# Optimization experiments

Hardware: AMD Instinct MI355X
Metric: run time of the kernel (lower is better)

## Reference

```python
import jax, jax.numpy as jnp
import numpy as np

B, T, C = 2, 2048, 1024
HS = 64              # head_size
H = C // HS          # 16 heads
DW, DA, DV, DG = 64, 64, 32, 160   # RWKV-7 LoRA dims for C=1024
FFN = 4 * C
GN_EPS = 64e-5       # ln_x GroupNorm eps from source


def _layernorm(h, w, b, eps=1e-5):
    mu = jnp.mean(h, axis=-1, keepdims=True)
    var = jnp.mean(jnp.square(h - mu), axis=-1, keepdims=True)
    return (h - mu) * jax.lax.rsqrt(var + eps) * w + b


def _time_shift_delta(h):
    # ZeroPad2d((0,0,1,-1))(h) - h : previous-token delta
    return jnp.pad(h, ((0, 0), (1, 0), (0, 0)))[:, :-1, :] - h


def _wkv7_scan(decay, r, k, v, a, b, S0):
    # all inputs [B,T,H,N]; state S [B,H,N_v,N_k]
    # S_t = S_{t-1} * diag(decay_t) + (S_{t-1} @ a_t) b_t^T + v_t k_t^T ; y_t = S_t @ r_t
    def step(S, inp):
        w_t, r_t, k_t, v_t, a_t, b_t = inp
        S = S * w_t[:, :, None, :]
        sa = jnp.einsum('bhij,bhj->bhi', S, a_t)
        S = S + sa[..., None] * b_t[:, :, None, :] + v_t[..., None] * k_t[:, :, None, :]
        y = jnp.einsum('bhij,bhj->bhi', S, r_t)
        return S, y
    seq = tuple(jnp.moveaxis(t, 1, 0) for t in (decay, r, k, v, a, b))
    S_last, y = jax.lax.scan(step, S0, seq)
    return jnp.moveaxis(y, 0, 1), S_last


def _block_forward(x, v_first, init_state, ln1_w, ln1_b, ln2_w, ln2_b,
                   x_r, x_w, x_k, x_v, x_a, x_g, w0, w1, w2, a0, a1, a2,
                   v0, v1, v2, g1, g2, k_k, k_a, r_k, W_r, W_k, W_v, W_o,
                   ln_x_w, ln_x_b, mix_k_ffn, W_key_ffn, W_val_ffn):
    # ---- time-mix (RWKV_Tmix_x070), layer_idx = 1 ----
    xn = _layernorm(x, ln1_w, ln1_b)
    xx = _time_shift_delta(xn)
    xr = xn + xx * x_r
    xw = xn + xx * x_w
    xk = xn + xx * x_k
    xv = xn + xx * x_v
    xa = xn + xx * x_a
    xg = xn + xx * x_g
    r = xr @ W_r.T
    w = -jax.nn.softplus(-(w0 + jnp.tanh(xw @ w1) @ w2)) - 0.5   # w <= -0.5
    k = xk @ W_k.T
    v = xv @ W_v.T
    v = v + (v_first - v) * jax.nn.sigmoid(v0 + (xv @ v1) @ v2)  # layer_idx > 0 path
    a = jax.nn.sigmoid(a0 + (xa @ a1) @ a2)
    g = jax.nn.sigmoid(xg @ g1) @ g2
    kk = (k * k_k).reshape(B, T, H, HS)
    kk = kk / jnp.maximum(jnp.linalg.norm(kk, axis=-1, keepdims=True), 1e-12)
    k = k * (1.0 + (a - 1.0) * k_a)
    r4 = r.reshape(B, T, H, HS)
    k4 = k.reshape(B, T, H, HS)
    v4 = v.reshape(B, T, H, HS)
    a4 = a.reshape(B, T, H, HS)
    decay = jnp.exp(w).reshape(B, T, H, HS)
    y, S_last = _wkv7_scan(decay, r4, k4, v4, -kk, kk * a4, init_state)
    # GroupNorm(H groups, eps=64e-5) over C, per (b,t)
    mu = jnp.mean(y, axis=-1, keepdims=True)
    var = jnp.mean(jnp.square(y - mu), axis=-1, keepdims=True)
    y = ((y - mu) * jax.lax.rsqrt(var + GN_EPS)).reshape(B, T, C) * ln_x_w + ln_x_b
    y = y + (jnp.sum(r4 * k4 * r_k, axis=-1, keepdims=True) * v4).reshape(B, T, C)
    x = x + (y * g) @ W_o.T
    # ---- channel-mix (RWKV_CMix_x070) ----
    xn2 = _layernorm(x, ln2_w, ln2_b)
    kf = xn2 + _time_shift_delta(xn2) * mix_k_ffn
    kf = jnp.square(jax.nn.relu(kf @ W_key_ffn.T))
    x = x + kf @ W_val_ffn.T
    return x, v_first


def setup_inputs():
    key = jax.random.key(0)
    ks = iter(jax.random.split(key, 40))
    def nrm(shape, s):
        return jax.random.normal(next(ks), shape, dtype=jnp.float32) * s
    def uni(shape, lo=0.0, hi=1.0):
        return jax.random.uniform(next(ks), shape, dtype=jnp.float32, minval=lo, maxval=hi)
    return {
        'x': nrm((B, T, C), 1.0),
        'v_first': nrm((B, T, C), 1.0),
        'init_state': jnp.zeros((B, H, HS, HS), jnp.float32),
        'ln1_w': jnp.ones((C,), jnp.float32), 'ln1_b': jnp.zeros((C,), jnp.float32),
        'ln2_w': jnp.ones((C,), jnp.float32), 'ln2_b': jnp.zeros((C,), jnp.float32),
        'x_r': uni((C,)), 'x_w': uni((C,)), 'x_k': uni((C,)),
        'x_v': uni((C,)), 'x_a': uni((C,)), 'x_g': uni((C,)),
        'w0': uni((C,), -6.5, -1.5),
        'w1': nrm((C, DW), 0.02), 'w2': nrm((DW, C), 0.02),
        'a0': jnp.zeros((C,), jnp.float32),
        'a1': nrm((C, DA), 0.02), 'a2': nrm((DA, C), 0.02),
        'v0': jnp.ones((C,), jnp.float32),
        'v1': nrm((C, DV), 0.02), 'v2': nrm((DV, C), 0.02),
        'g1': nrm((C, DG), 0.02), 'g2': nrm((DG, C), 0.02),
        'k_k': 0.85 * jnp.ones((C,), jnp.float32),
        'k_a': jnp.ones((C,), jnp.float32),
        'r_k': nrm((H, HS), 0.02),
        'W_r': nrm((C, C), 0.02), 'W_k': nrm((C, C), 0.02),
        'W_v': nrm((C, C), 0.02), 'W_o': nrm((C, C), 0.02),
        'ln_x_w': jnp.ones((C,), jnp.float32), 'ln_x_b': jnp.zeros((C,), jnp.float32),
        'mix_k_ffn': uni((C,)),
        'W_key_ffn': nrm((FFN, C), 0.02), 'W_val_ffn': nrm((C, FFN), 0.02),
    }


def reference(x, v_first, init_state, ln1_w, ln1_b, ln2_w, ln2_b,
              x_r, x_w, x_k, x_v, x_a, x_g, w0, w1, w2, a0, a1, a2,
              v0, v1, v2, g1, g2, k_k, k_a, r_k, W_r, W_k, W_v, W_o,
              ln_x_w, ln_x_b, mix_k_ffn, W_key_ffn, W_val_ffn):
    return _block_forward(x, v_first, init_state, ln1_w, ln1_b, ln2_w, ln2_b,
                          x_r, x_w, x_k, x_v, x_a, x_g, w0, w1, w2, a0, a1, a2,
                          v0, v1, v2, g1, g2, k_k, k_a, r_k, W_r, W_k, W_v, W_o,
                          ln_x_w, ln_x_b, mix_k_ffn, W_key_ffn, W_val_ffn)
```

## Files before the change

kernel.cpp:

```cpp
#include <hip/hip_runtime.h>
#include <math.h>

#define Bb 2
#define Tt 2048
#define Cc 1024
#define Hh 16
#define BT 4096
#define FFNd 4096
#define CH 16
#define CL 128
#define WU 32
#define BIGN 3456
#define BIGK 2048
#define LORAK 320
#define BIGW 4096

typedef __attribute__((ext_vector_type(8))) short bf16x8;
typedef __attribute__((ext_vector_type(4))) float f32x4;
typedef unsigned short u16;

__device__ __forceinline__ float sgm(float x){ return 1.0f/(1.0f+expf(-x)); }

template<int MAXM>
__device__ __forceinline__ float redgrp(float v){
  #pragma unroll
  for (int m=1; m<=MAXM; m<<=1) v += __shfl_xor(v, m, 64);
  return v;
}

template<int CTRL>
__device__ __forceinline__ float dppadd(float v){
  union { float f; int i; } u, r;
  u.f = v;
  r.i = __builtin_amdgcn_update_dpp(u.i, u.i, CTRL, 0xf, 0xf, true);
  return v + r.f;
}
__device__ __forceinline__ float red16(float v){
  v = dppadd<0xB1>(v);
  v = dppadd<0x4E>(v);
  v = dppadd<0x141>(v);
  v = dppadd<0x140>(v);
  return v;
}

__device__ __forceinline__ unsigned pack_bf16(float a, float b){
  unsigned ua = __builtin_bit_cast(unsigned, a);
  unsigned ub = __builtin_bit_cast(unsigned, b);
  ua = (ua + 0x7FFFu + ((ua>>16)&1u)) >> 16;
  ub = (ub + 0x7FFFu + ((ub>>16)&1u)) >> 16;
  return ua | (ub<<16);
}
__device__ __forceinline__ u16 bf16_1(float a){
  unsigned ua = __builtin_bit_cast(unsigned, a);
  return (u16)((ua + 0x7FFFu + ((ua>>16)&1u)) >> 16);
}

__device__ __forceinline__ void gload16(const void* g, void* l){
  __builtin_amdgcn_global_load_lds(
    (const __attribute__((address_space(1))) unsigned int*)g,
    (__attribute__((address_space(3))) unsigned int*)l, 16, 0, 0);
}

__device__ __forceinline__ void cvt8(const float* __restrict__ in,
    u16* __restrict__ out, size_t i){
  float4 a = ((const float4*)in)[2*i];
  float4 b = ((const float4*)in)[2*i+1];
  uint4 o = {pack_bf16(a.x,a.y), pack_bf16(a.z,a.w),
             pack_bf16(b.x,b.y), pack_bf16(b.z,b.w)};
  ((uint4*)out)[i] = o;
}
__global__ __launch_bounds__(256) void cvtall_kernel(
    const float* __restrict__ wo, u16* __restrict__ wob,
    const float* __restrict__ wk, u16* __restrict__ wkb,
    const float* __restrict__ wv, u16* __restrict__ wvb,
    const float* __restrict__ csrc, float* __restrict__ cdst) {
  size_t i = (size_t)blockIdx.x*256 + threadIdx.x;
  const size_t NA = (size_t)Cc*Cc/8;
  const size_t NB = (size_t)FFNd*Cc/8;
  if (i < NA) cvt8(wo, wob, i);
  else if (i < NA+NB) cvt8(wk, wkb, i-NA);
  else if (i < NA+2*NB) cvt8(wv, wvb, i-NA-NB);
  else {
    size_t j = i - NA - 2*NB;
    float4 a = ((const float4*)csrc)[2*j];
    float4 b = ((const float4*)csrc)[2*j+1];
    ((float4*)cdst)[2*j] = a;
    ((float4*)cdst)[2*j+1] = b;
  }
}

__global__ __launch_bounds__(256) void packW_kernel(const float* __restrict__ Wr,
    const float* __restrict__ Wk, const float* __restrict__ Wv,
    const float* __restrict__ xr, const float* __restrict__ xk,
    const float* __restrict__ xv, u16* __restrict__ out) {
  int which = blockIdx.y;
  const float* W   = which==0 ? Wr : (which==1 ? Wk : Wv);
  const float* mix = which==0 ? xr : (which==1 ? xk : xv);
  u16* o = out + (size_t)which*1024*BIGK;
  int n = blockIdx.x;
  int c0 = threadIdx.x*8;
  int ks = c0 & 1023;
  const float* src = W + (size_t)n*Cc + ks;
  float4 a = *(const float4*)src;
  float4 b = *(const float4*)(src+4);
  if (c0 >= 1024){
    float4 m0 = *(const float4*)(mix + ks);
    float4 m1 = *(const float4*)(mix + ks + 4);
    a.x*=m0.x; a.y*=m0.y; a.z*=m0.z; a.w*=m0.w;
    b.x*=m1.x; b.y*=m1.y; b.z*=m1.z; b.w*=m1.w;
  }
  uint4 ov = {pack_bf16(a.x,a.y), pack_bf16(a.z,a.w),
              pack_bf16(b.x,b.y), pack_bf16(b.z,b.w)};
  *(uint4*)(o + (size_t)n*BIGK + c0) = ov;
}

__global__ __launch_bounds__(256) void packL_kernel(const float* __restrict__ w1,
    const float* __restrict__ a1, const float* __restrict__ v1,
    const float* __restrict__ g1, const float* __restrict__ x_w,
    const float* __restrict__ x_a, const float* __restrict__ x_v,
    const float* __restrict__ x_g, u16* __restrict__ out) {
  int bid = blockIdx.x;
  const float* W1; const float* mix; int D, d, nbase;
  if (bid < 64)       { W1=w1; mix=x_w; D=64;  d=bid;     nbase=3072; }
  else if (bid < 128) { W1=a1; mix=x_a; D=64;  d=bid-64;  nbase=3136; }
  else if (bid < 160) { W1=v1; mix=x_v; D=32;  d=bid-128; nbase=3200; }
  else                { W1=g1; mix=x_g; D=160; d=bid-160; nbase=3232; }
  int k0 = threadIdx.x*8;
  float v[8];
  #pragma unroll
  for (int q=0;q<8;++q){
    int kk = k0+q;
    int ks = kk & 1023;
    float t = W1[(size_t)ks*D + d];
    if (kk >= 1024) t *= mix[ks];
    v[q] = t;
  }
  uint4 o = {pack_bf16(v[0],v[1]), pack_bf16(v[2],v[3]),
             pack_bf16(v[4],v[5]), pack_bf16(v[6],v[7])};
  *(uint4*)(out + (size_t)(nbase+d)*BIGK + k0) = o;
}

__global__ __launch_bounds__(320) void packW2_kernel(const float* __restrict__ w2,
    const float* __restrict__ a2, const float* __restrict__ v2,
    const float* __restrict__ g2, u16* __restrict__ out) {
  int n = blockIdx.x; int k = threadIdx.x;
  int which = n >> 10, col = n & 1023;
  float v = 0.f;
  if (which==0)      { if (k < 64)              v = w2[(size_t)k*Cc + col]; }
  else if (which==1) { if (k >= 64 && k < 128)  v = a2[(size_t)(k-64)*Cc + col]; }
  else if (which==2) { if (k >= 128 && k < 160) v = v2[(size_t)(k-128)*Cc + col]; }
  else               { if (k >= 160)            v = g2[(size_t)(k-160)*Cc + col]; }
  out[(size_t)n*LORAK + k] = bf16_1(v);
}

__global__ __launch_bounds__(320) void actcvt_kernel(const float* __restrict__ m,
    u16* __restrict__ loraAct) {
  int i = blockIdx.x; int cc = threadIdx.x;
  float v = m[(size_t)i*BIGN + 3072 + cc];
  if (cc < 64) v = tanhf(v);
  else if (cc >= 160) v = sgm(v);
  loraAct[(size_t)i*LORAK + cc] = bf16_1(v);
}

__global__ __launch_bounds__(256) void lnmix1_kernel(const float* __restrict__ x,
    const float* __restrict__ w, const float* __restrict__ b,
    u16* __restrict__ bigA) {
  int rowg = blockIdx.x; int t = rowg & (Tt-1);
  int tid = threadIdx.x;
  size_t off = (size_t)rowg*Cc + tid*4;
  float4 vc = *(const float4*)(x + off);
  float4 vp = {0.f,0.f,0.f,0.f};
  if (t) vp = *(const float4*)(x + off - Cc);
  float sc = vc.x+vc.y+vc.z+vc.w;
  float qc = vc.x*vc.x+vc.y*vc.y+vc.z*vc.z+vc.w*vc.w;
  float sp = vp.x+vp.y+vp.z+vp.w;
  float qp = vp.x*vp.x+vp.y*vp.y+vp.z*vp.z+vp.w*vp.w;
  sc = redgrp<32>(sc); qc = redgrp<32>(qc);
  sp = redgrp<32>(sp); qp = redgrp<32>(qp);
  __shared__ float rbuf[4][4];
  int lane = tid & 63, wv = tid >> 6;
  if (lane==0){ rbuf[wv][0]=sc; rbuf[wv][1]=qc; rbuf[wv][2]=sp; rbuf[wv][3]=qp; }
  __syncthreads();
  sc = rbuf[0][0]+rbuf[1][0]+rbuf[2][0]+rbuf[3][0];
  qc = rbuf[0][1]+rbuf[1][1]+rbuf[2][1]+rbuf[3][1];
  sp = rbuf[0][2]+rbuf[1][2]+rbuf[2][2]+rbuf[3][2];
  qp = rbuf[0][3]+rbuf[1][3]+rbuf[2][3]+rbuf[3][3];
  float muc = sc*(1.0f/Cc), mup = sp*(1.0f/Cc);
  float rnc = rsqrtf(qc*(1.0f/Cc) - muc*muc + 1e-5f);
  float rnp = rsqrtf(qp*(1.0f/Cc) - mup*mup + 1e-5f);
  float4 w4 = *(const float4*)(w + tid*4);
  float4 b4 = *(const float4*)(b + tid*4);
  float vcl[4]={vc.x,vc.y,vc.z,vc.w};
  float vpl[4]={vp.x,vp.y,vp.z,vp.w};
  float wl[4]={w4.x,w4.y,w4.z,w4.w};
  float bl[4]={b4.x,b4.y,b4.z,b4.w};
  float xnc[4], xx[4];
  #pragma unroll
  for (int q=0;q<4;++q){
    xnc[q] = (vcl[q]-muc)*rnc*wl[q] + bl[q];
    float xnp = t ? ((vpl[q]-mup)*rnp*wl[q] + bl[q]) : 0.0f;
    xx[q] = xnp - xnc[q];
  }
  size_t ab = (size_t)rowg*BIGK + tid*4;
  uint2 p0 = {pack_bf16(xnc[0],xnc[1]), pack_bf16(xnc[2],xnc[3])};
  uint2 p1 = {pack_bf16(xx[0],xx[1]),   pack_bf16(xx[2],xx[3])};
  *(uint2*)(bigA + ab) = p0;
  *(uint2*)(bigA + ab + 1024) = p1;
}

__global__ __launch_bounds__(256) void lnmix2_kernel(const float* __restrict__ x,
    const float* __restrict__ w, const float* __restrict__ b,
    const float* __restrict__ mixk, u16* __restrict__ outb) {
  int rowg = blockIdx.x; int t = rowg & (Tt-1);
  int tid = threadIdx.x;
  size_t off = (size_t)rowg*Cc + tid*4;
  float4 vc = *(const float4*)(x + off);
  float4 vp = {0.f,0.f,0.f,0.f};
  if (t) vp = *(const float4*)(x + off - Cc);
  float sc = vc.x+vc.y+vc.z+vc.w;
  float qc = vc.x*vc.x+vc.y*vc.y+vc.z*vc.z+vc.w*vc.w;
  float sp = vp.x+vp.y+vp.z+vp.w;
  float qp = vp.x*vp.x+vp.y*vp.y+vp.z*vp.z+vp.w*vp.w;
  sc = redgrp<32>(sc); qc = redgrp<32>(qc);
  sp = redgrp<32>(sp); qp = redgrp<32>(qp);
  __shared__ float rbuf[4][4];
  int lane = tid & 63, wv = tid >> 6;
  if (lane==0){ rbuf[wv][0]=sc; rbuf[wv][1]=qc; rbuf[wv][2]=sp; rbuf[wv][3]=qp; }
  __syncthreads();
  sc = rbuf[0][0]+rbuf[1][0]+rbuf[2][0]+rbuf[3][0];
  qc = rbuf[0][1]+rbuf[1][1]+rbuf[2][1]+rbuf[3][1];
  sp = rbuf[0][2]+rbuf[1][2]+rbuf[2][2]+rbuf[3][2];
  qp = rbuf[0][3]+rbuf[1][3]+rbuf[2][3]+rbuf[3][3];
  float muc = sc*(1.0f/Cc), mup = sp*(1.0f/Cc);
  float rnc = rsqrtf(qc*(1.0f/Cc) - muc*muc + 1e-5f);
  float rnp = rsqrtf(qp*(1.0f/Cc) - mup*mup + 1e-5f);
  float4 w4 = *(const float4*)(w + tid*4);
  float4 b4 = *(const float4*)(b + tid*4);
  float4 m = *(const float4*)(mixk + tid*4);
  float vcl[4]={vc.x,vc.y,vc.z,vc.w};
  float vpl[4]={vp.x,vp.y,vp.z,vp.w};
  float wl[4]={w4.x,w4.y,w4.z,w4.w};
  float bl[4]={b4.x,b4.y,b4.z,b4.w};
  float ml[4]={m.x,m.y,m.z,m.w};
  float o[4];
  #pragma unroll
  for (int q=0;q<4;++q){
    float xnc = (vcl[q]-muc)*rnc*wl[q] + bl[q];
    float xnp = t ? ((vpl[q]-mup)*rnp*wl[q] + bl[q]) : 0.0f;
    o[q] = xnc + (xnp - xnc)*ml[q];
  }
  uint2 p = {pack_bf16(o[0],o[1]), pack_bf16(o[2],o[3])};
  *(uint2*)(outb + off) = p;
}

template<int MODE, int BN>
__global__ __launch_bounds__(256) void gemm_bf16(const u16* __restrict__ A,
    const u16* __restrict__ W, void* __restrict__ outv,
    const float* __restrict__ res, int M, int N, int K) {
  constexpr int NJ = BN/32;
  constexpr int NBCH = BN/32;
  __shared__ u16 As[2][128*64];
  __shared__ u16 Bs[2][BN*64];
  int tid = threadIdx.x;
  int nwg = gridDim.x;
  int q8 = nwg >> 3;
  int id = (blockIdx.x & 7)*q8 + (blockIdx.x >> 3);
  int nbx = N / BN;
  int bm = id / nbx, bn = id - bm*nbx;
  int wave = tid >> 6, lane = tid & 63;
  int wm = wave >> 1, wn = wave & 1;
  int srowA = wave*32 + (lane>>3);
  int srowB = wave*(BN/4) + (lane>>3);
  int scol = (((lane&7) ^ ((lane>>3)&7)))*8;
  const u16* Ag = A + (size_t)(bm*128 + srowA)*K + scol;
  const u16* Wg = W + (size_t)(bn*BN + srowB)*K + scol;
  int nt = K >> 6;
  f32x4 acc[4][NJ];
  f32x4 zero = {0.f,0.f,0.f,0.f};
  #pragma unroll
  for (int i=0;i<4;++i)
    #pragma unroll
    for (int j=0;j<NJ;++j) acc[i][j] = zero;

  #define STAGE(buf, t) { \
    const u16* Ag2 = Ag + (size_t)(t)*64; \
    const u16* Wg2 = Wg + (size_t)(t)*64; \
    _Pragma("unroll") \
    for (int i_=0;i_<4;++i_) \
      gload16(Ag2 + (size_t)i_*8*K, &As[buf][(wave*32+i_*8)*64]); \
    _Pragma("unroll") \
    for (int i_=0;i_<NBCH;++i_) \
      gload16(Wg2 + (size_t)i_*8*K, &Bs[buf][(wave*(BN/4)+i_*8)*64]); }

  STAGE(0, 0);
  int lrow = lane & 15, lk8 = lane >> 4;
  int r7 = lrow & 7;
  for (int t = 0; t < nt; ++t) {
    int cur = t & 1;
    if (t+1 < nt) {
      STAGE(cur^1, t+1);
      if (BN == 128) asm volatile("s_waitcnt vmcnt(8)\n\ts_barrier" ::: "memory");
      else           asm volatile("s_waitcnt vmcnt(6)\n\ts_barrier" ::: "memory");
    } else {
      asm volatile("s_waitcnt vmcnt(0)\n\ts_barrier" ::: "memory");
    }
    #pragma unroll
    for (int kk2 = 0; kk2 < 2; ++kk2) {
      int sl = ((kk2*4 + lk8) ^ r7) * 8;
      bf16x8 af[4], bfr[NJ];
      #pragma unroll
      for (int i=0;i<4;++i)
        af[i] = *(const bf16x8*)&As[cur][(wm*64 + i*16 + lrow)*64 + sl];
      #pragma unroll
      for (int j=0;j<NJ;++j)
        bfr[j] = *(const bf16x8*)&Bs[cur][(wn*(BN/2) + j*16 + lrow)*64 + sl];
      #pragma unroll
      for (int i=0;i<4;++i)
        #pragma unroll
        for (int j=0;j<NJ;++j)
          acc[i][j] = __builtin_amdgcn_mfma_f32_16x16x32_bf16(af[i], bfr[j], acc[i][j], 0, 0, 0);
    }
    asm volatile("s_barrier" ::: "memory");
  }
  #undef STAGE
  float* outf = (float*)outv;
  u16* outb = (u16*)outv;
  int crow4 = (lane>>4)*4, ccol = lane & 15;
  #pragma unroll
  for (int i=0;i<4;++i){
    #pragma unroll
    for (int j=0;j<NJ;++j){
      int gr = bm*128 + wm*64 + i*16 + crow4;
      int gc = bn*BN + wn*(BN/2) + j*16 + ccol;
      #pragma unroll
      for (int q=0;q<4;++q){
        float v = acc[i][j][q];
        size_t o = (size_t)(gr+q)*N + gc;
        if (MODE==1) { v += res[o]; outf[o] = v; }
        else if (MODE==2) { v = fmaxf(v, 0.f); outb[o] = bf16_1(v*v); }
        else outf[o] = v;
      }
    }
  }
}

__global__ __launch_bounds__(256) void prep_kernel(
    const float* __restrict__ kraw, const float* __restrict__ dw,
    const float* __restrict__ da, const float* __restrict__ dv,
    const float* __restrict__ vraw, const float* __restrict__ vfirst,
    const float* __restrict__ w0, const float* __restrict__ a0,
    const float* __restrict__ v0, const float* __restrict__ k_k,
    const float* __restrict__ k_a,
    float* __restrict__ decay, float* __restrict__ kfin, float* __restrict__ vfin,
    float* __restrict__ Ak, float* __restrict__ Bk) {
  int row = blockIdx.x; int tid = threadIdx.x; int c = tid*4;
  size_t off = (size_t)row*Cc + c;
  size_t offw = (size_t)row*BIGN + c;
  size_t offd = (size_t)row*BIGW + c;
  float4 kr = *(const float4*)(kraw+offw);
  float4 vr = *(const float4*)(vraw+offw);
  float4 w4 = *(const float4*)(dw+offd);
  float4 A4 = *(const float4*)(da+offd);
  float4 V4 = *(const float4*)(dv+offd);
  float4 vf = *(const float4*)(vfirst+off);
  float4 w04 = *(const float4*)(w0+c);
  float4 a04 = *(const float4*)(a0+c);
  float4 v04 = *(const float4*)(v0+c);
  float4 kk4 = *(const float4*)(k_k+c);
  float4 ka4 = *(const float4*)(k_a+c);
  float krl[4]={kr.x,kr.y,kr.z,kr.w};
  float dwl[4]={w4.x,w4.y,w4.z,w4.w};
  float dal[4]={A4.x,A4.y,A4.z,A4.w};
  float dvl[4]={V4.x,V4.y,V4.z,V4.w};
  float vrl[4]={vr.x,vr.y,vr.z,vr.w};
  float vfl[4]={vf.x,vf.y,vf.z,vf.w};
  float w0l[4]={w04.x,w04.y,w04.z,w04.w};
  float a0l[4]={a04.x,a04.y,a04.z,a04.w};
  float v0l[4]={v04.x,v04.y,v04.z,v04.w};
  float kkl[4]={kk4.x,kk4.y,kk4.z,kk4.w};
  float kal[4]={ka4.x,ka4.y,ka4.z,ka4.w};
  float av[4], dec[4], vv[4], kp[4], kf[4];
  float ss = 0.f;
  #pragma unroll
  for (int q=0;q<4;++q){
    av[q] = sgm(a0l[q] + dal[q]);
    dec[q] = 0.60653065971263342f * sgm(w0l[q] + dwl[q]);
    float sv = sgm(v0l[q] + dvl[q]);
    vv[q] = vrl[q] + (vfl[q]-vrl[q])*sv;
    kp[q] = krl[q]*kkl[q];
    ss += kp[q]*kp[q];
    kf[q] = krl[q]*(1.0f + (av[q]-1.0f)*kal[q]);
  }
  ss = redgrp<8>(ss);
  float inv = 1.0f / fmaxf(sqrtf(ss), 1e-12f);
  float4 o;
  o.x=dec[0];o.y=dec[1];o.z=dec[2];o.w=dec[3];  *(float4*)(decay+off)=o;
  o.x=kf[0]; o.y=kf[1]; o.z=kf[2]; o.w=kf[3];   *(float4*)(kfin+off)=o;
  o.x=vv[0]; o.y=vv[1]; o.z=vv[2]; o.w=vv[3];   *(float4*)(vfin+off)=o;
  o.x=-kp[0]*inv; o.y=-kp[1]*inv; o.z=-kp[2]*inv; o.w=-kp[3]*inv; *(float4*)(Ak+off)=o;
  o.x=kp[0]*inv*av[0]; o.y=kp[1]*inv*av[1]; o.z=kp[2]*inv*av[2]; o.w=kp[3]*inv*av[3];
  *(float4*)(Bk+off)=o;
}

__global__ __launch_bounds__(512) void wkv_kernel(
    const float* __restrict__ decay, const float* __restrict__ Ak,
    const float* __restrict__ Bk, const float* __restrict__ kfin,
    const float* __restrict__ r_, const float* __restrict__ vfin,
    const float* __restrict__ S0, float* __restrict__ y) {
  __shared__ float lds[2][6][CH][64];
  int bid = blockIdx.x;
  int bh = bid & 31, c = bid >> 5;
  int bb = bh >> 4, h = bh & 15;
  int tid = threadIdx.x;
  int wave = tid >> 6, lane = tid & 63;
  int rg = tid >> 4;
  int bj = tid & 15, j0 = bj*4;
  int r0 = rg, r1 = rg + 32;
  float Sa_[4] = {0.f,0.f,0.f,0.f};
  float Sb_[4] = {0.f,0.f,0.f,0.f};
  if (c == 0) {
    float4 t0 = *(const float4*)(S0 + (size_t)bh*4096 + r0*64 + j0);
    float4 t1 = *(const float4*)(S0 + (size_t)bh*4096 + r1*64 + j0);
    Sa_[0]=t0.x; Sa_[1]=t0.y; Sa_[2]=t0.z; Sa_[3]=t0.w;
    Sb_[0]=t1.x; Sb_[1]=t1.y; Sb_[2]=t1.z; Sb_[3]=t1.w;
  }
  size_t seqb = (size_t)bb*Tt;
  int t0g = (c==0) ? 0 : (c*CL - WU);
  int NPH = (c==0) ? (CL/CH) : ((CL+WU)/CH);
  int phE = (c==0) ? 0 : (WU/CH);
  int lhi = lane >> 4, llo4 = (lane & 15)*4;

  #define WST1(buf, stepb, arr, base, ldv) { \
    const float* gp_ = (base) + (size_t)(seqb + (size_t)(stepb) + lhi)*(ldv) + h*64 + llo4; \
    _Pragma("unroll") \
    for (int p_=0; p_<4; ++p_) \
      gload16(gp_ + (size_t)p_*4*(ldv), &lds[buf][arr][p_*4][0]); }
  #define WSTAGE(buf, stepb) { \
    if (wave==0)      { WST1(buf, stepb, 0, decay, Cc) } \
    else if (wave==1) { WST1(buf, stepb, 1, Ak, Cc) } \
    else if (wave==2) { WST1(buf, stepb, 2, Bk, Cc) } \
    else if (wave==3) { WST1(buf, stepb, 3, kfin, Cc) } \
    else if (wave==4) { WST1(buf, stepb, 4, r_, BIGN) } \
    else if (wave==5) { WST1(buf, stepb, 5, vfin, Cc) } }

  WSTAGE(0, t0g);
  for (int ph = 0; ph < NPH; ++ph) {
    int cur = ph & 1;
    if (ph+1 < NPH) {
      WSTAGE(cur^1, t0g + (ph+1)*CH);
      asm volatile("s_waitcnt vmcnt(4)\n\ts_barrier" ::: "memory");
    } else {
      asm volatile("s_waitcnt vmcnt(0)\n\ts_barrier" ::: "memory");
    }
    bool emit = (ph >= phE);
    const float* L0 = &lds[cur][0][0][0];
    #pragma unroll
    for (int s = 0; s < CH; ++s) {
      const float* bp = L0 + s*64;
      float4 d4 = *(const float4*)(bp + 0*CH*64 + j0);
      float4 a4 = *(const float4*)(bp + 1*CH*64 + j0);
      float4 b4 = *(const float4*)(bp + 2*CH*64 + j0);
      float4 k4 = *(const float4*)(bp + 3*CH*64 + j0);
      float4 r4 = *(const float4*)(bp + 4*CH*64 + j0);
      float v0 = bp[5*CH*64 + r0];
      float v1 = bp[5*CH*64 + r1];
      Sa_[0]*=d4.x; Sa_[1]*=d4.y; Sa_[2]*=d4.z; Sa_[3]*=d4.w;
      Sb_[0]*=d4.x; Sb_[1]*=d4.y; Sb_[2]*=d4.z; Sb_[3]*=d4.w;
      float sa0 = fmaf(Sa_[0],a4.x, Sa_[1]*a4.y) + fmaf(Sa_[2],a4.z, Sa_[3]*a4.w);
      float sa1 = fmaf(Sb_[0],a4.x, Sb_[1]*a4.y) + fmaf(Sb_[2],a4.z, Sb_[3]*a4.w);
      sa0 = red16(sa0);
      sa1 = red16(sa1);
      Sa_[0]=fmaf(v0,k4.x,Sa_[0]); Sa_[1]=fmaf(v0,k4.y,Sa_[1]);
      Sa_[2]=fmaf(v0,k4.z,Sa_[2]); Sa_[3]=fmaf(v0,k4.w,Sa_[3]);
      Sa_[0]=fmaf(sa0,b4.x,Sa_[0]); Sa_[1]=fmaf(sa0,b4.y,Sa_[1]);
      Sa_[2]=fmaf(sa0,b4.z,Sa_[2]); Sa_[3]=fmaf(sa0,b4.w,Sa_[3]);
      Sb_[0]=fmaf(v1,k4.x,Sb_[0]); Sb_[1]=fmaf(v1,k4.y,Sb_[1]);
      Sb_[2]=fmaf(v1,k4.z,Sb_[2]); Sb_[3]=fmaf(v1,k4.w,Sb_[3]);
      Sb_[0]=fmaf(sa1,b4.x,Sb_[0]); Sb_[1]=fmaf(sa1,b4.y,Sb_[1]);
      Sb_[2]=fmaf(sa1,b4.z,Sb_[2]); Sb_[3]=fmaf(sa1,b4.w,Sb_[3]);
      if (emit) {
        float y0 = fmaf(Sa_[0],r4.x, Sa_[1]*r4.y) + fmaf(Sa_[2],r4.z, Sa_[3]*r4.w);
        float y1 = fmaf(Sb_[0],r4.x, Sb_[1]*r4.y) + fmaf(Sb_[2],r4.z, Sb_[3]*r4.w);
        y0 = red16(y0);
        y1 = red16(y1);
        if (bj == 0) {
          size_t yo = (seqb + (size_t)t0g + ph*CH + s)*Cc + h*64;
          y[yo + r0] = y0;
          y[yo + r1] = y1;
        }
      }
    }
    asm volatile("s_barrier" ::: "memory");
  }
  #undef WSTAGE
  #undef WST1
}

__global__ __launch_bounds__(256) void gn_kernel(
    const float* __restrict__ y, const float* __restrict__ r_,
    const float* __restrict__ kfin, const float* __restrict__ vfin,
    const float* __restrict__ g_, const float* __restrict__ lnxw,
    const float* __restrict__ lnxb, const float* __restrict__ r_k,
    u16* __restrict__ Ao) {
  int row = blockIdx.x; int tid = threadIdx.x; int c = tid*4;
  size_t off = (size_t)row*Cc + c;
  float4 y4 = *(const float4*)(y+off);
  float s = y4.x+y4.y+y4.z+y4.w;
  float q = y4.x*y4.x+y4.y*y4.y+y4.z*y4.z+y4.w*y4.w;
  s = redgrp<8>(s); q = redgrp<8>(q);
  float mu = s*(1.0f/64.0f);
  float var = q*(1.0f/64.0f) - mu*mu;
  float rn = rsqrtf(var + 64e-5f);
  float4 rr = *(const float4*)(r_ + (size_t)row*BIGN + c);
  float4 kk = *(const float4*)(kfin+off);
  float4 vv = *(const float4*)(vfin+off);
  float4 gg = *(const float4*)(g_ + (size_t)row*BIGW + c);
  int h = tid >> 4; int hs = (tid & 15)*4;
  float4 rk = *(const float4*)(r_k + h*64 + hs);
  float dp = rr.x*kk.x*rk.x + rr.y*kk.y*rk.y + rr.z*kk.z*rk.z + rr.w*kk.w*rk.w;
  dp = redgrp<8>(dp);
  float4 w4 = *(const float4*)(lnxw+c);
  float4 b4 = *(const float4*)(lnxb+c);
  float o0 = (((y4.x-mu)*rn)*w4.x + b4.x + dp*vv.x) * gg.x;
  float o1 = (((y4.y-mu)*rn)*w4.y + b4.y + dp*vv.y) * gg.y;
  float o2 = (((y4.z-mu)*rn)*w4.z + b4.z + dp*vv.z) * gg.z;
  float o3 = (((y4.w-mu)*rn)*w4.w + b4.w + dp*vv.w) * gg.w;
  uint2 p = {pack_bf16(o0,o1), pack_bf16(o2,o3)};
  *(uint2*)(Ao + off) = p;
}

extern "C" void kernel_launch(void* const* d_in, const int* in_sizes, int n_in,
                              void* d_out, int out_size, void* d_ws, size_t ws_size,
                              hipStream_t stream) {
  const float* x      = (const float*)d_in[0];
  const float* vfirst = (const float*)d_in[1];
  const float* S0     = (const float*)d_in[2];
  const float* ln1w   = (const float*)d_in[3];
  const float* ln1b   = (const float*)d_in[4];
  const float* ln2w   = (const float*)d_in[5];
  const float* ln2b   = (const float*)d_in[6];
  const float* x_r    = (const float*)d_in[7];
  const float* x_w    = (const float*)d_in[8];
  const float* x_k    = (const float*)d_in[9];
  const float* x_v    = (const float*)d_in[10];
  const float* x_a    = (const float*)d_in[11];
  const float* x_g    = (const float*)d_in[12];
  const float* w0     = (const float*)d_in[13];
  const float* w1     = (const float*)d_in[14];
  const float* w2     = (const float*)d_in[15];
  const float* a0     = (const float*)d_in[16];
  const float* a1     = (const float*)d_in[17];
  const float* a2     = (const float*)d_in[18];
  const float* v0     = (const float*)d_in[19];
  const float* v1     = (const float*)d_in[20];
  const float* v2     = (const float*)d_in[21];
  const float* g1     = (const float*)d_in[22];
  const float* g2     = (const float*)d_in[23];
  const float* k_k    = (const float*)d_in[24];
  const float* k_a    = (const float*)d_in[25];
  const float* r_k    = (const float*)d_in[26];
  const float* W_r    = (const float*)d_in[27];
  const float* W_k    = (const float*)d_in[28];
  const float* W_v    = (const float*)d_in[29];
  const float* W_o    = (const float*)d_in[30];
  const float* lnxw   = (const float*)d_in[31];
  const float* lnxb   = (const float*)d_in[32];
  const float* mixk   = (const float*)d_in[33];
  const float* Wkey   = (const float*)d_in[34];
  const float* Wval   = (const float*)d_in[35];
  float* out = (float*)d_out;
  float* ws  = (float*)d_ws;
  const size_t U = (size_t)BT * Cc;
  float* u[14];
  for (int i=0;i<14;++i) u[i] = ws + i*U;

  u16* bigA   = (u16*)u[0];
  u16* BigB   = (u16*)u[1];
  float* bigOut = u[2];
  float* dwdavg = u[6];
  u16* W2blk  = (u16*)u[10];
  u16* loraAct= (u16*)u[11];
  float* Bk   = u[0];
  float* y_   = u[1];
  u16* gnb    = (u16*)u[10];
  u16* Wob    = (u16*)u[13];
  float* xo   = u[0];
  u16* Wkeyb  = (u16*)u[6];
  u16* cmb    = (u16*)u[7];
  u16* Wvalb  = (u16*)u[8];
  u16* midb   = (u16*)u[2];

  dim3 b256(256);
  packW_kernel<<<dim3(Cc,3), b256, 0, stream>>>(W_r, W_k, W_v, x_r, x_k, x_v, BigB);
  packL_kernel<<<320, b256, 0, stream>>>(w1, a1, v1, g1, x_w, x_a, x_v, x_g, BigB);
  packW2_kernel<<<BIGW, dim3(320), 0, stream>>>(w2, a2, v2, g2, W2blk);
  lnmix1_kernel<<<BT, b256, 0, stream>>>(x, ln1w, ln1b, bigA);
  gemm_bf16<0,128><<<(BT/128)*(BIGN/128), b256, 0, stream>>>(bigA, BigB, bigOut, nullptr, BT, BIGN, BIGK);
  actcvt_kernel<<<BT, dim3(320), 0, stream>>>(bigOut, loraAct);
  gemm_bf16<0,128><<<(BT/128)*(BIGW/128), b256, 0, stream>>>(loraAct, W2blk, dwdavg, nullptr, BT, BIGW, LORAK);
  prep_kernel<<<BT, b256, 0, stream>>>(bigOut+1024, dwdavg, dwdavg+1024, dwdavg+2048,
      bigOut+2048, vfirst, w0, a0, v0, k_k, k_a, u[10], u[11], u[12], u[13], Bk);
  wkv_kernel<<<32*(Tt/CL), dim3(512), 0, stream>>>(u[10], u[13], Bk, u[11], bigOut, u[12], S0, y_);
  gn_kernel<<<BT, b256, 0, stream>>>(y_, bigOut, u[11], u[12], dwdavg+3072, lnxw, lnxb, r_k, gnb);
  cvtall_kernel<<<(Cc*Cc + FFNd*Cc*2 + BT*Cc)/2048, b256, 0, stream>>>(
      W_o, Wob, Wkey, Wkeyb, Wval, Wvalb, vfirst, out + (size_t)BT*Cc);
  gemm_bf16<1,64><<<(BT/128)*(Cc/64), b256, 0, stream>>>(gnb, Wob, xo, x, BT, Cc, Cc);
  lnmix2_kernel<<<BT, b256, 0, stream>>>(xo, ln2w, ln2b, mixk, cmb);
  gemm_bf16<2,128><<<(BT/128)*(FFNd/128), b256, 0, stream>>>(cmb, Wkeyb, midb, nullptr, BT, FFNd, Cc);
  gemm_bf16<1,64><<<(BT/128)*(Cc/64), b256, 0, stream>>>(midb, Wvalb, out, xo, BT, Cc, FFNd);
}
```

Before: 394.2 us.

## Add 256x256-tile 8-wave GEMM for fused projection and FFN key GEMMs

Introduces a 512-thread GEMM kernel with 256x256 output tiles and double-buffered LDS. Its schedule interleaves global prefetch of the next K tile with MFMA quadrants, separated by barriers, and raises wave priority around the MFMA blocks. The fused r/k/v/LoRA projection and the FFN key GEMM switch to this kernel to get more data reuse per tile and fewer global loads. To fit the 256-wide tiles, the fused projection width is padded up, which adds extra padded compute, and each GEMM now launches fewer, larger workgroups.

```diff
diff --git a/kernel.cpp b/kernel.cpp
--- a/kernel.cpp
+++ b/kernel.cpp
@@ -10,7 +10,7 @@
 #define CH 16
 #define CL 128
 #define WU 32
-#define BIGN 3456
+#define BIGN 3584
 #define BIGK 2048
 #define LORAK 320
 #define BIGW 4096
@@ -251,6 +251,133 @@
   }
   uint2 p = {pack_bf16(o[0],o[1]), pack_bf16(o[2],o[3])};
   *(uint2*)(outb + off) = p;
+}
+
+template<int MODE>
+__global__ __launch_bounds__(512) void gemm8(const u16* __restrict__ A,
+    const u16* __restrict__ W, void* __restrict__ outv, int M, int N, int K) {
+  __shared__ u16 As[2*2*128*64];
+  __shared__ u16 Bs[2*2*128*64];
+  int tid = threadIdx.x;
+  int nwg = gridDim.x;
+  int q8 = nwg >> 3;
+  int id = (blockIdx.x & 7)*q8 + (blockIdx.x >> 3);
+  int nbx = N >> 8;
+  int bm = id / nbx, bn = id - bm*nbx;
+  int wave = tid >> 6, lane = tid & 63;
+  int wm = wave >> 2, wn = wave & 3;
+  int lrow = lane & 15, lk8 = lane >> 4;
+  int r7 = lrow & 7;
+  int bhlf = wn >> 1;
+  int chb = (wn & 1)*64;
+  int sw = wave*16;
+  int sl8 = lane >> 3;
+  int schunk = ((lane & 7) ^ sl8) * 8;
+  int nt = K >> 6;
+  int lastJ = (nt >> 1) - 1;
+  f32x4 acc[8][4];
+  f32x4 zero = {0.f,0.f,0.f,0.f};
+  #pragma unroll
+  for (int i=0;i<8;++i)
+    #pragma unroll
+    for (int j=0;j<4;++j) acc[i][j] = zero;
+
+  #define STGA(T, h) { \
+    const u16* s_ = A + (size_t)(bm*256 + (h)*128 + sw + sl8)*K + (size_t)(T)*64 + schunk; \
+    char* d_ = (char*)As + (((T)&1)*32768 + (h)*16384) + wave*2048; \
+    gload16(s_, d_); \
+    gload16(s_ + (size_t)8*K, d_ + 1024); }
+  #define STGB(T, h) { \
+    const u16* s_ = W + (size_t)(bn*256 + (h)*128 + sw + sl8)*K + (size_t)(T)*64 + schunk; \
+    char* d_ = (char*)Bs + (((T)&1)*32768 + (h)*16384) + wave*2048; \
+    gload16(s_, d_); \
+    gload16(s_ + (size_t)8*K, d_ + 1024); }
+  #define RDA(T, mh) { \
+    _Pragma("unroll") \
+    for (int ii=0; ii<4; ++ii) \
+      _Pragma("unroll") \
+      for (int kk=0; kk<2; ++kk) \
+        Am[ii][kk] = *(const bf16x8*)&As[((T)&1)*16384 + wm*8192 + \
+          ((mh)*64 + ii*16 + lrow)*64 + ((kk*4 + lk8) ^ r7)*8]; }
+  #define RDB(T, nh, Bd) { \
+    _Pragma("unroll") \
+    for (int jj=0; jj<2; ++jj) \
+      _Pragma("unroll") \
+      for (int kk=0; kk<2; ++kk) \
+        Bd[jj][kk] = *(const bf16x8*)&Bs[((T)&1)*16384 + bhlf*8192 + \
+          (chb + ((nh)*2+jj)*16 + lrow)*64 + ((kk*4 + lk8) ^ r7)*8]; }
+  #define QMM(mh, nh, Bd) { \
+    __builtin_amdgcn_s_setprio(1); \
+    _Pragma("unroll") \
+    for (int ii=0; ii<4; ++ii) \
+      _Pragma("unroll") \
+      for (int jj=0; jj<2; ++jj) \
+        _Pragma("unroll") \
+        for (int kk=0; kk<2; ++kk) \
+          acc[(mh)*4+ii][(nh)*2+jj] = __builtin_amdgcn_mfma_f32_16x16x32_bf16( \
+            Am[ii][kk], Bd[jj][kk], acc[(mh)*4+ii][(nh)*2+jj], 0, 0, 0); \
+    __builtin_amdgcn_s_setprio(0); }
+
+  bf16x8 Am[4][2], B0f[2][2], B1f[2][2];
+  STGA(0,0); STGA(0,1); STGB(0,0); STGB(0,1); STGA(1,0);
+  for (int J = 0; J <= lastJ; ++J) {
+    int T0 = 2*J, T1 = 2*J+1;
+    bool more = (J < lastJ);
+    asm volatile("s_waitcnt vmcnt(2)\n\ts_barrier" ::: "memory");
+    RDA(T0, 0); RDB(T0, 0, B0f);
+    STGA(T1, 1);
+    QMM(0, 0, B0f);
+    asm volatile("s_barrier" ::: "memory");
+    RDB(T0, 1, B1f);
+    STGB(T1, 0);
+    QMM(0, 1, B1f);
+    asm volatile("s_barrier" ::: "memory");
+    RDA(T0, 1);
+    STGB(T1, 1);
+    QMM(1, 0, B0f);
+    asm volatile("s_barrier" ::: "memory");
+    if (more) STGA(T0+2, 0);
+    QMM(1, 1, B1f);
+    if (more) asm volatile("s_waitcnt vmcnt(2)\n\ts_barrier" ::: "memory");
+    else      asm volatile("s_waitcnt vmcnt(0)\n\ts_barrier" ::: "memory");
+    RDA(T1, 0); RDB(T1, 0, B0f);
+    if (more) STGA(T0+2, 1);
+    QMM(0, 0, B0f);
+    asm volatile("s_barrier" ::: "memory");
+    RDB(T1, 1, B1f);
+    if (more) STGB(T0+2, 0);
+    QMM(0, 1, B1f);
+    asm volatile("s_barrier" ::: "memory");
+    RDA(T1, 1);
+    if (more) STGB(T0+2, 1);
+    QMM(1, 0, B0f);
+    asm volatile("s_barrier" ::: "memory");
+    if (more) STGA(T0+3, 0);
+    QMM(1, 1, B1f);
+  }
+  #undef STGA
+  #undef STGB
+  #undef RDA
+  #undef RDB
+  #undef QMM
+  float* outf = (float*)outv;
+  u16* outb = (u16*)outv;
+  int crow4 = (lane>>4)*4, ccol = lane & 15;
+  #pragma unroll
+  for (int i=0;i<8;++i){
+    #pragma unroll
+    for (int j=0;j<4;++j){
+      int gr = bm*256 + wm*128 + i*16 + crow4;
+      int gc = bn*256 + wn*64 + j*16 + ccol;
+      #pragma unroll
+      for (int q=0;q<4;++q){
+        float v = acc[i][j][q];
+        size_t o = (size_t)(gr+q)*N + gc;
+        if (MODE==2) { v = fmaxf(v, 0.f); outb[o] = bf16_1(v*v); }
+        else outf[o] = v;
+      }
+    }
+  }
 }
 
 template<int MODE, int BN>
@@ -595,7 +722,7 @@
   packL_kernel<<<320, b256, 0, stream>>>(w1, a1, v1, g1, x_w, x_a, x_v, x_g, BigB);
   packW2_kernel<<<BIGW, dim3(320), 0, stream>>>(w2, a2, v2, g2, W2blk);
   lnmix1_kernel<<<BT, b256, 0, stream>>>(x, ln1w, ln1b, bigA);
-  gemm_bf16<0,128><<<(BT/128)*(BIGN/128), b256, 0, stream>>>(bigA, BigB, bigOut, nullptr, BT, BIGN, BIGK);
+  gemm8<0><<<(BT/256)*(BIGN/256), dim3(512), 0, stream>>>(bigA, BigB, bigOut, BT, BIGN, BIGK);
   actcvt_kernel<<<BT, dim3(320), 0, stream>>>(bigOut, loraAct);
   gemm_bf16<0,128><<<(BT/128)*(BIGW/128), b256, 0, stream>>>(loraAct, W2blk, dwdavg, nullptr, BT, BIGW, LORAK);
   prep_kernel<<<BT, b256, 0, stream>>>(bigOut+1024, dwdavg, dwdavg+1024, dwdavg+2048,
@@ -606,6 +733,6 @@
       W_o, Wob, Wkey, Wkeyb, Wval, Wvalb, vfirst, out + (size_t)BT*Cc);
   gemm_bf16<1,64><<<(BT/128)*(Cc/64), b256, 0, stream>>>(gnb, Wob, xo, x, BT, Cc, Cc);
   lnmix2_kernel<<<BT, b256, 0, stream>>>(xo, ln2w, ln2b, mixk, cmb);
-  gemm_bf16<2,128><<<(BT/128)*(FFNd/128), b256, 0, stream>>>(cmb, Wkeyb, midb, nullptr, BT, FFNd, Cc);
+  gemm8<2><<<(BT/256)*(FFNd/256), dim3(512), 0, stream>>>(cmb, Wkeyb, midb, BT, FFNd, Cc);
   gemm_bf16<1,64><<<(BT/128)*(Cc/64), b256, 0, stream>>>(midb, Wvalb, out, xo, BT, Cc, FFNd);
 }
```

After: 377.1 us. 1.05x faster.
